# Kernel optimization log

Hardware: AMD Instinct MI355X
Metric: run time of the kernel (lower is better)

The kernel has to match this reference:

```python
import jax, jax.numpy as jnp
import numpy as np

N = 8192
IN_F = 512
OUT_F = 128
ALPHA = 0.2  # leaky relu negative slope
NEG_BIG = -1e10
RND_SCALE = 1e5


def setup_inputs() -> dict:
    key = jax.random.key(0)
    k1, k2, k3, k4, k5 = jax.random.split(key, 5)
    h = jax.random.normal(k1, (N, IN_F), dtype=jnp.float32)
    adj = jax.random.randint(k2, (N, N), 0, 2, dtype=jnp.int32)
    W = jax.random.normal(k3, (IN_F, OUT_F), dtype=jnp.float32) * 0.05
    a = jax.random.normal(k4, (2 * OUT_F, 1), dtype=jnp.float32) * 0.1
    # rnd in original is 1e5*(rand-0.5); same distribution here
    rnd = RND_SCALE * (jax.random.uniform(k5, (N, OUT_F), dtype=jnp.float32) - 0.5)
    return {"h": h, "adj": adj, "W": W, "a": a, "rnd": rnd}


def reference(h, adj, W, a, rnd):
    Wh = h @ W                              # [N, OUT_F]
    Wh1 = Wh @ a[:OUT_F, :]                 # [N, 1]
    Wh2 = Wh @ a[OUT_F:, :]                 # [N, 1]
    e = jax.nn.leaky_relu(Wh1 + Wh2.T, negative_slope=ALPHA)  # [N, N]
    attention = jnp.where(adj > 0, e, NEG_BIG)
    attention = jax.nn.softmax(attention, axis=1)
    h_prime = attention @ Wh                # [N, OUT_F]
    h_prime = (h_prime + rnd) / RND_SCALE
    return jax.nn.elu(h_prime)
```

## Files before the change

kernel.cpp:

```cpp
#include <hip/hip_runtime.h>

#define N 8192
#define IN_F 512
#define OUT_F 128
#define NW (N / 8)
#define SPLITK 16
#define LOG2E 1.4426950408889634f
#define LN2 0.6931471805599453f

typedef __attribute__((ext_vector_type(4))) float f32x4;
typedef __attribute__((ext_vector_type(8))) short bf16x8;

__device__ __forceinline__ short f2bf(float f) {
    union { float f; unsigned u; } c; c.f = f;
    unsigned r = c.u + 0x7FFFu + ((c.u >> 16) & 1u);
    return (short)(r >> 16);
}

__device__ __forceinline__ float exp2fast(float x) {
#if __has_builtin(__builtin_amdgcn_exp2f)
    return __builtin_amdgcn_exp2f(x);
#else
    return __expf(x * LN2);
#endif
}

__global__ __launch_bounds__(256) void conv_W(const float* __restrict__ W, short* __restrict__ WT) {
    int idx = blockIdx.x * 256 + threadIdx.x;
    int n = idx & (OUT_F - 1);
    int k = idx >> 7;
    WT[(size_t)n * IN_F + k] = f2bf(W[idx]);
}

__global__ __launch_bounds__(256) void mkmask(const int* __restrict__ adj,
                                              unsigned char* __restrict__ maskR) {
    const int wave = threadIdx.x >> 6, lane = threadIdx.x & 63;
    const size_t m = (size_t)blockIdx.x * 4 + wave;
    const int4* ap = (const int4*)(adj + m * N);
    unsigned char* mp = maskR + m * NW;
#pragma unroll 4
    for (int it = 0; it < 16; it++) {
        int b4 = it * 128 + lane * 2;
        int4 a0 = ap[b4], a1 = ap[b4 + 1];
        unsigned b = (unsigned)(a0.x > 0) | ((unsigned)(a0.y > 0) << 1) |
                     ((unsigned)(a0.z > 0) << 2) | ((unsigned)(a0.w > 0) << 3) |
                     ((unsigned)(a1.x > 0) << 4) | ((unsigned)(a1.y > 0) << 5) |
                     ((unsigned)(a1.z > 0) << 6) | ((unsigned)(a1.w > 0) << 7);
        mp[it * 64 + lane] = (unsigned char)b;
    }
}

__global__ __launch_bounds__(256) void gemm_hW(const float* __restrict__ h,
                                               const short* __restrict__ WT,
                                               const float* __restrict__ a,
                                               short* __restrict__ WhT,
                                               float* __restrict__ sOut,
                                               float* __restrict__ tOut) {
    const int tid = threadIdx.x;
    const int wave = tid >> 6, lane = tid & 63;
    const int row16 = lane & 15, kgrp = lane >> 4;
    const int m0 = blockIdx.x * 16;
    const int kbase = wave * 128;

    f32x4 acc[8] = {};
    const float4* hp = (const float4*)(h + (size_t)(m0 + row16) * IN_F + kbase);

#pragma unroll
    for (int kk = 0; kk < 128; kk += 32) {
        float4 u0 = hp[kk / 4 + kgrp * 2];
        float4 u1 = hp[kk / 4 + kgrp * 2 + 1];
        bf16x8 af;
        af[0] = f2bf(u0.x); af[1] = f2bf(u0.y); af[2] = f2bf(u0.z); af[3] = f2bf(u0.w);
        af[4] = f2bf(u1.x); af[5] = f2bf(u1.y); af[6] = f2bf(u1.z); af[7] = f2bf(u1.w);
#pragma unroll
        for (int nt = 0; nt < 8; nt++) {
            bf16x8 bf_ = *(const bf16x8*)(WT + (size_t)(nt * 16 + row16) * IN_F + kbase + kk + kgrp * 8);
            acc[nt] = __builtin_amdgcn_mfma_f32_16x16x32_bf16(af, bf_, acc[nt], 0, 0, 0);
        }
    }

    __shared__ float red[4][16][132];
#pragma unroll
    for (int nt = 0; nt < 8; nt++)
#pragma unroll
        for (int r = 0; r < 4; r++)
            red[wave][kgrp * 4 + r][nt * 16 + row16] = acc[nt][r];
    __syncthreads();

    const int row = tid >> 4, seg = tid & 15;
    float v[8];
#pragma unroll
    for (int e = 0; e < 8; e++) {
        int c = seg * 8 + e;
        v[e] = red[0][row][c] + red[1][row][c] + red[2][row][c] + red[3][row][c];
    }
    float sp = 0.f, tp = 0.f;
#pragma unroll
    for (int e = 0; e < 8; e++) {
        sp += v[e] * a[seg * 8 + e];
        tp += v[e] * a[OUT_F + seg * 8 + e];
    }
    sp += __shfl_xor(sp, 1); tp += __shfl_xor(tp, 1);
    sp += __shfl_xor(sp, 2); tp += __shfl_xor(tp, 2);
    sp += __shfl_xor(sp, 4); tp += __shfl_xor(tp, 4);
    sp += __shfl_xor(sp, 8); tp += __shfl_xor(tp, 8);
    if (seg == 0) {
        sOut[m0 + row] = sp * LOG2E;
        tOut[m0 + row] = tp * LOG2E;
    }
#pragma unroll
    for (int e = 0; e < 8; e++)
        WhT[(size_t)(seg * 8 + e) * N + m0 + row] = f2bf(v[e]);
}

__global__ __launch_bounds__(512, 2) void attn(const unsigned char* __restrict__ maskR,
                                               const short* __restrict__ WhT,
                                               const float* __restrict__ s,
                                               const float* __restrict__ t,
                                               float* __restrict__ num,
                                               float* __restrict__ lpart) {
    const int tid = threadIdx.x;
    const int wave = tid >> 6, lane = tid & 63;
    const int row16 = lane & 15, kgrp = lane >> 4;
    const int m0 = blockIdx.x * 512 + wave * 64;
    const int ks = blockIdx.y * 512;

    __shared__ float tl[512];
    if (tid < 512) tl[tid] = t[ks + tid];
    __syncthreads();

    float s_m[4];
    const unsigned long long* mrow[4];
#pragma unroll
    for (int mi = 0; mi < 4; mi++) {
        int m = m0 + mi * 16 + row16;
        s_m[mi] = s[m];
        mrow[mi] = (const unsigned long long*)(maskR + (size_t)m * NW + (ks >> 3));
    }

    f32x4 acc[4][8] = {};
    float lsum[4] = {0.f, 0.f, 0.f, 0.f};

    unsigned long long mcur[4], mnxt[4];
#pragma unroll
    for (int mi = 0; mi < 4; mi++) { mcur[mi] = mrow[mi][0]; mnxt[mi] = mrow[mi][1]; }

    for (int c2 = 0; c2 < 8; c2++) {
        unsigned long long mk[4];
#pragma unroll
        for (int mi = 0; mi < 4; mi++) { mk[mi] = mcur[mi]; mcur[mi] = mnxt[mi]; }
        if (c2 < 6) {
#pragma unroll
            for (int mi = 0; mi < 4; mi++) mnxt[mi] = mrow[mi][c2 + 2];
        }
#pragma unroll
        for (int cc = 0; cc < 2; cc++) {
            const int k0 = c2 * 64 + cc * 32;
            const float* tp = tl + k0 + kgrp * 8;
            float4 tA = *(const float4*)tp;
            float4 tB = *(const float4*)(tp + 4);
            float tv[8] = { tA.x, tA.y, tA.z, tA.w, tB.x, tB.y, tB.z, tB.w };

            bf16x8 bfr[8];
            const short* bb = WhT + ks + k0 + kgrp * 8;
#pragma unroll
            for (int ni = 0; ni < 8; ni++)
                bfr[ni] = *(const bf16x8*)(bb + (size_t)(ni * 16 + row16) * N);

#pragma unroll
            for (int mi = 0; mi < 4; mi++) {
                unsigned bbyte = (unsigned)(mk[mi] >> (cc * 32 + kgrp * 8)) & 0xFFu;
                unsigned pu[8];
#pragma unroll
                for (int e = 0; e < 8; e++) {
                    float x = s_m[mi] + tv[e];
                    x = fmaxf(x, 0.2f * x);
                    float p = exp2fast(x);
                    unsigned u = __float_as_uint(p) & 0xFFFF0000u;
                    u = ((bbyte >> e) & 1u) ? u : 0u;
                    lsum[mi] += __uint_as_float(u);
                    pu[e] = u;
                }
                bf16x8 af;
                unsigned* au = (unsigned*)&af;
#pragma unroll
                for (int q = 0; q < 4; q++) au[q] = (pu[2 * q] >> 16) | pu[2 * q + 1];
#pragma unroll
                for (int ni = 0; ni < 8; ni++)
                    acc[mi][ni] = __builtin_amdgcn_mfma_f32_16x16x32_bf16(af, bfr[ni], acc[mi][ni], 0, 0, 0);
            }
        }
    }

#pragma unroll
    for (int mi = 0; mi < 4; mi++) {
        float v = lsum[mi];
        v += __shfl_xor(v, 16);
        v += __shfl_xor(v, 32);
        if (kgrp == 0) lpart[(size_t)blockIdx.y * N + m0 + mi * 16 + row16] = v;
    }

    float* np_ = num + (size_t)blockIdx.y * N * OUT_F;
#pragma unroll
    for (int mi = 0; mi < 4; mi++) {
        int mb = m0 + mi * 16 + kgrp * 4;
#pragma unroll
        for (int ni = 0; ni < 8; ni++) {
            int n = ni * 16 + row16;
#pragma unroll
            for (int r = 0; r < 4; r++)
                np_[(size_t)(mb + r) * OUT_F + n] = acc[mi][ni][r];
        }
    }
}

__global__ __launch_bounds__(256) void finalize(const float* __restrict__ num,
                                                const float* __restrict__ lpart,
                                                const float* __restrict__ rnd,
                                                float* __restrict__ out) {
    int idx = blockIdx.x * 256 + threadIdx.x;
    int m = idx >> 7;
    float l = 0.f, nm = 0.f;
#pragma unroll
    for (int bk = 0; bk < SPLITK; bk++) {
        l  += lpart[bk * N + m];
        nm += num[(size_t)bk * N * OUT_F + idx];
    }
    float hp = nm / fmaxf(l, 1e-30f);
    float x = (hp + rnd[idx]) * 1e-5f;
    out[idx] = x > 0.f ? x : __expf(x) - 1.f;
}

extern "C" void kernel_launch(void* const* d_in, const int* in_sizes, int n_in,
                              void* d_out, int out_size, void* d_ws, size_t ws_size,
                              hipStream_t stream) {
    const float* h   = (const float*)d_in[0];
    const int*   adj = (const int*)d_in[1];
    const float* W   = (const float*)d_in[2];
    const float* a   = (const float*)d_in[3];
    const float* rnd = (const float*)d_in[4];
    float* out = (float*)d_out;

    char* w = (char*)d_ws;
    short* WT    = (short*)(w);
    short* WhT   = (short*)(w + 131072);
    float* sv    = (float*)(w + 2228224);
    float* tv    = (float*)(w + 2260992);
    float* lpart = (float*)(w + 2293760);
    unsigned char* maskR = (unsigned char*)(w + 2818048);
    float* num   = (float*)(w + 11206656);

    conv_W  <<<256, 256, 0, stream>>>(W, WT);
    mkmask  <<<2048, 256, 0, stream>>>(adj, maskR);
    gemm_hW <<<512, 256, 0, stream>>>(h, WT, a, WhT, sv, tv);
    attn    <<<dim3(16, SPLITK), 512, 0, stream>>>(maskR, WhT, sv, tv, num, lpart);
    finalize<<<(N * OUT_F) / 256, 256, 0, stream>>>(num, lpart, rnd, out);
}
```

Before: 446.9 us.

## Read adjacency directly in attention kernel, drop mask pass, store partials as bf16

Removes the separate bitmask-building kernel, so the attention kernel now streams the int32 adjacency matrix itself through a two-deep register prefetch. Each wave now covers 32 rows instead of 64, doubling the grid to 512 blocks. Split-K numerator partials are written as bf16 instead of fp32, and the finalize kernel is vectorised to process 8 outputs per thread. The intent is to avoid writing and re-reading the mask and to halve partial-sum traffic. In exchange the attention kernel reads 256MB of adjacency directly, reuses each WhT fragment across fewer rows, and bf16 partials lose some precision.

```diff
diff --git a/kernel.cpp b/kernel.cpp
--- a/kernel.cpp
+++ b/kernel.cpp
@@ -3,13 +3,13 @@
 #define N 8192
 #define IN_F 512
 #define OUT_F 128
-#define NW (N / 8)
 #define SPLITK 16
 #define LOG2E 1.4426950408889634f
 #define LN2 0.6931471805599453f
 
 typedef __attribute__((ext_vector_type(4))) float f32x4;
 typedef __attribute__((ext_vector_type(8))) short bf16x8;
+typedef __attribute__((ext_vector_type(8))) unsigned short u16x8;
 
 __device__ __forceinline__ short f2bf(float f) {
     union { float f; unsigned u; } c; c.f = f;
@@ -30,24 +30,6 @@
     int n = idx & (OUT_F - 1);
     int k = idx >> 7;
     WT[(size_t)n * IN_F + k] = f2bf(W[idx]);
-}
-
-__global__ __launch_bounds__(256) void mkmask(const int* __restrict__ adj,
-                                              unsigned char* __restrict__ maskR) {
-    const int wave = threadIdx.x >> 6, lane = threadIdx.x & 63;
-    const size_t m = (size_t)blockIdx.x * 4 + wave;
-    const int4* ap = (const int4*)(adj + m * N);
-    unsigned char* mp = maskR + m * NW;
-#pragma unroll 4
-    for (int it = 0; it < 16; it++) {
-        int b4 = it * 128 + lane * 2;
-        int4 a0 = ap[b4], a1 = ap[b4 + 1];
-        unsigned b = (unsigned)(a0.x > 0) | ((unsigned)(a0.y > 0) << 1) |
-                     ((unsigned)(a0.z > 0) << 2) | ((unsigned)(a0.w > 0) << 3) |
-                     ((unsigned)(a1.x > 0) << 4) | ((unsigned)(a1.y > 0) << 5) |
-                     ((unsigned)(a1.z > 0) << 6) | ((unsigned)(a1.w > 0) << 7);
-        mp[it * 64 + lane] = (unsigned char)b;
-    }
 }
 
 __global__ __launch_bounds__(256) void gemm_hW(const float* __restrict__ h,
@@ -113,122 +95,146 @@
         WhT[(size_t)(seg * 8 + e) * N + m0 + row] = f2bf(v[e]);
 }
 
-__global__ __launch_bounds__(512, 2) void attn(const unsigned char* __restrict__ maskR,
+__global__ __launch_bounds__(512, 2) void attn(const int* __restrict__ adj,
                                                const short* __restrict__ WhT,
                                                const float* __restrict__ s,
                                                const float* __restrict__ t,
-                                               float* __restrict__ num,
+                                               unsigned short* __restrict__ num,
                                                float* __restrict__ lpart) {
     const int tid = threadIdx.x;
     const int wave = tid >> 6, lane = tid & 63;
     const int row16 = lane & 15, kgrp = lane >> 4;
-    const int m0 = blockIdx.x * 512 + wave * 64;
+    const int m0 = blockIdx.x * 256 + wave * 32;
     const int ks = blockIdx.y * 512;
 
     __shared__ float tl[512];
     if (tid < 512) tl[tid] = t[ks + tid];
     __syncthreads();
 
-    float s_m[4];
-    const unsigned long long* mrow[4];
-#pragma unroll
-    for (int mi = 0; mi < 4; mi++) {
+    float s_m[2];
+    const int4* ap[2];
+#pragma unroll
+    for (int mi = 0; mi < 2; mi++) {
         int m = m0 + mi * 16 + row16;
         s_m[mi] = s[m];
-        mrow[mi] = (const unsigned long long*)(maskR + (size_t)m * NW + (ks >> 3));
-    }
-
-    f32x4 acc[4][8] = {};
-    float lsum[4] = {0.f, 0.f, 0.f, 0.f};
-
-    unsigned long long mcur[4], mnxt[4];
-#pragma unroll
-    for (int mi = 0; mi < 4; mi++) { mcur[mi] = mrow[mi][0]; mnxt[mi] = mrow[mi][1]; }
-
-    for (int c2 = 0; c2 < 8; c2++) {
-        unsigned long long mk[4];
-#pragma unroll
-        for (int mi = 0; mi < 4; mi++) { mk[mi] = mcur[mi]; mcur[mi] = mnxt[mi]; }
-        if (c2 < 6) {
-#pragma unroll
-            for (int mi = 0; mi < 4; mi++) mnxt[mi] = mrow[mi][c2 + 2];
-        }
-#pragma unroll
-        for (int cc = 0; cc < 2; cc++) {
-            const int k0 = c2 * 64 + cc * 32;
-            const float* tp = tl + k0 + kgrp * 8;
-            float4 tA = *(const float4*)tp;
-            float4 tB = *(const float4*)(tp + 4);
-            float tv[8] = { tA.x, tA.y, tA.z, tA.w, tB.x, tB.y, tB.z, tB.w };
-
-            bf16x8 bfr[8];
-            const short* bb = WhT + ks + k0 + kgrp * 8;
+        ap[mi] = (const int4*)(adj + (size_t)m * N + ks) + kgrp * 2;
+    }
+
+    f32x4 acc[2][8] = {};
+    float lsum[2] = {0.f, 0.f};
+
+    int4 buf[2][2][2];
+#pragma unroll
+    for (int mi = 0; mi < 2; mi++)
+#pragma unroll
+        for (int q = 0; q < 2; q++) {
+            buf[0][mi][q] = ap[mi][q];
+            buf[1][mi][q] = ap[mi][8 + q];
+        }
+
+#pragma unroll 2
+    for (int c = 0; c < 16; c++) {
+        int4 cur[2][2];
+#pragma unroll
+        for (int mi = 0; mi < 2; mi++)
+#pragma unroll
+            for (int q = 0; q < 2; q++) cur[mi][q] = buf[c & 1][mi][q];
+        if (c < 14) {
+#pragma unroll
+            for (int mi = 0; mi < 2; mi++)
+#pragma unroll
+                for (int q = 0; q < 2; q++) buf[c & 1][mi][q] = ap[mi][(c + 2) * 8 + q];
+        }
+
+        const float* tp = tl + c * 32 + kgrp * 8;
+        float4 tA = *(const float4*)tp;
+        float4 tB = *(const float4*)(tp + 4);
+        float tv[8] = { tA.x, tA.y, tA.z, tA.w, tB.x, tB.y, tB.z, tB.w };
+
+        bf16x8 bfr[8];
+        const short* bb = WhT + ks + c * 32 + kgrp * 8;
+#pragma unroll
+        for (int ni = 0; ni < 8; ni++)
+            bfr[ni] = *(const bf16x8*)(bb + (size_t)(ni * 16 + row16) * N);
+
+#pragma unroll
+        for (int mi = 0; mi < 2; mi++) {
+            const int* ai = (const int*)cur[mi];
+            unsigned pu[8];
+#pragma unroll
+            for (int e = 0; e < 8; e++) {
+                float x = s_m[mi] + tv[e];
+                x = fmaxf(x, 0.2f * x);
+                float p = exp2fast(x);
+                unsigned u = __float_as_uint(p) & 0xFFFF0000u;
+                u = ai[e] > 0 ? u : 0u;
+                lsum[mi] += __uint_as_float(u);
+                pu[e] = u;
+            }
+            bf16x8 af;
+            unsigned* au = (unsigned*)&af;
+#pragma unroll
+            for (int q = 0; q < 4; q++) au[q] = (pu[2 * q] >> 16) | pu[2 * q + 1];
 #pragma unroll
             for (int ni = 0; ni < 8; ni++)
-                bfr[ni] = *(const bf16x8*)(bb + (size_t)(ni * 16 + row16) * N);
-
-#pragma unroll
-            for (int mi = 0; mi < 4; mi++) {
-                unsigned bbyte = (unsigned)(mk[mi] >> (cc * 32 + kgrp * 8)) & 0xFFu;
-                unsigned pu[8];
-#pragma unroll
-                for (int e = 0; e < 8; e++) {
-                    float x = s_m[mi] + tv[e];
-                    x = fmaxf(x, 0.2f * x);
-                    float p = exp2fast(x);
-                    unsigned u = __float_as_uint(p) & 0xFFFF0000u;
-                    u = ((bbyte >> e) & 1u) ? u : 0u;
-                    lsum[mi] += __uint_as_float(u);
-                    pu[e] = u;
-                }
-                bf16x8 af;
-                unsigned* au = (unsigned*)&af;
-#pragma unroll
-                for (int q = 0; q < 4; q++) au[q] = (pu[2 * q] >> 16) | pu[2 * q + 1];
-#pragma unroll
-                for (int ni = 0; ni < 8; ni++)
-                    acc[mi][ni] = __builtin_amdgcn_mfma_f32_16x16x32_bf16(af, bfr[ni], acc[mi][ni], 0, 0, 0);
-            }
-        }
-    }
-
-#pragma unroll
-    for (int mi = 0; mi < 4; mi++) {
+                acc[mi][ni] = __builtin_amdgcn_mfma_f32_16x16x32_bf16(af, bfr[ni], acc[mi][ni], 0, 0, 0);
+        }
+    }
+
+#pragma unroll
+    for (int mi = 0; mi < 2; mi++) {
         float v = lsum[mi];
         v += __shfl_xor(v, 16);
         v += __shfl_xor(v, 32);
         if (kgrp == 0) lpart[(size_t)blockIdx.y * N + m0 + mi * 16 + row16] = v;
     }
 
-    float* np_ = num + (size_t)blockIdx.y * N * OUT_F;
-#pragma unroll
-    for (int mi = 0; mi < 4; mi++) {
+    unsigned short* np_ = num + (size_t)blockIdx.y * N * OUT_F;
+#pragma unroll
+    for (int mi = 0; mi < 2; mi++) {
         int mb = m0 + mi * 16 + kgrp * 4;
 #pragma unroll
         for (int ni = 0; ni < 8; ni++) {
             int n = ni * 16 + row16;
 #pragma unroll
             for (int r = 0; r < 4; r++)
-                np_[(size_t)(mb + r) * OUT_F + n] = acc[mi][ni][r];
-        }
-    }
-}
-
-__global__ __launch_bounds__(256) void finalize(const float* __restrict__ num,
+                np_[(size_t)(mb + r) * OUT_F + n] = (unsigned short)f2bf(acc[mi][ni][r]);
+        }
+    }
+}
+
+__global__ __launch_bounds__(256) void finalize(const unsigned short* __restrict__ num,
                                                 const float* __restrict__ lpart,
                                                 const float* __restrict__ rnd,
                                                 float* __restrict__ out) {
     int idx = blockIdx.x * 256 + threadIdx.x;
-    int m = idx >> 7;
-    float l = 0.f, nm = 0.f;
+    int m = idx >> 4;
+    int c = (idx & 15) * 8;
+    size_t g = (size_t)m * OUT_F + c;
+
+    float nm[8] = {};
 #pragma unroll
     for (int bk = 0; bk < SPLITK; bk++) {
-        l  += lpart[bk * N + m];
-        nm += num[(size_t)bk * N * OUT_F + idx];
-    }
-    float hp = nm / fmaxf(l, 1e-30f);
-    float x = (hp + rnd[idx]) * 1e-5f;
-    out[idx] = x > 0.f ? x : __expf(x) - 1.f;
+        u16x8 v = *(const u16x8*)(num + (size_t)bk * N * OUT_F + g);
+#pragma unroll
+        for (int e = 0; e < 8; e++) nm[e] += __uint_as_float((unsigned)v[e] << 16);
+    }
+    float l = 0.f;
+#pragma unroll
+    for (int bk = 0; bk < SPLITK; bk++) l += lpart[(size_t)bk * N + m];
+    float inv = 1.f / fmaxf(l, 1e-30f);
+
+    float4 r0 = *(const float4*)(rnd + g);
+    float4 r1 = *(const float4*)(rnd + g + 4);
+    float rv[8] = { r0.x, r0.y, r0.z, r0.w, r1.x, r1.y, r1.z, r1.w };
+    float ov[8];
+#pragma unroll
+    for (int e = 0; e < 8; e++) {
+        float x = (nm[e] * inv + rv[e]) * 1e-5f;
+        ov[e] = x > 0.f ? x : __expf(x) - 1.f;
+    }
+    *(float4*)(out + g)     = make_float4(ov[0], ov[1], ov[2], ov[3]);
+    *(float4*)(out + g + 4) = make_float4(ov[4], ov[5], ov[6], ov[7]);
 }
 
 extern "C" void kernel_launch(void* const* d_in, const int* in_sizes, int n_in,
@@ -247,12 +253,10 @@
     float* sv    = (float*)(w + 2228224);
     float* tv    = (float*)(w + 2260992);
     float* lpart = (float*)(w + 2293760);
-    unsigned char* maskR = (unsigned char*)(w + 2818048);
-    float* num   = (float*)(w + 11206656);
+    unsigned short* num = (unsigned short*)(w + 2818048);
 
     conv_W  <<<256, 256, 0, stream>>>(W, WT);
-    mkmask  <<<2048, 256, 0, stream>>>(adj, maskR);
     gemm_hW <<<512, 256, 0, stream>>>(h, WT, a, WhT, sv, tv);
-    attn    <<<dim3(16, SPLITK), 512, 0, stream>>>(maskR, WhT, sv, tv, num, lpart);
-    finalize<<<(N * OUT_F) / 256, 256, 0, stream>>>(num, lpart, rnd, out);
-}
+    attn    <<<dim3(32, SPLITK), 512, 0, stream>>>(adj, WhT, sv, tv, num, lpart);
+    finalize<<<(N * OUT_F / 8) / 256, 256, 0, stream>>>(num, lpart, rnd, out);
+}
```

New measurement: 457.0 us. +2.3%, slower.
